# Performance work log

Hardware: AMD Instinct MI355X
Metric: run time of the kernel (lower is better)

The kernel has to match this reference:

```python
import jax, jax.numpy as jnp
import numpy as np

N = 100000
IN_CH, HID_CH, OUT_CH = 128, 128, 64
E = 1600000


def gcn_layer(x, W, b, src, dst, num_nodes):
    """PyG GCNConv: add self-loops, symmetric deg^-1/2 normalization,
    x' = D^-1/2 (A+I) D^-1/2 (x W) + b."""
    # degrees including self-loops (deg = 1 + in-degree with unit edge weights)
    ones = jnp.ones(dst.shape[0], dtype=x.dtype)
    deg = jnp.ones(num_nodes, dtype=x.dtype).at[dst].add(ones)
    dinv = jax.lax.rsqrt(deg)
    h = x @ W  # [N, out_dim] -- transform before propagate (PyG order)
    # neighbor messages
    norm = dinv[src] * dinv[dst]                      # [E]
    msg = h[src] * norm[:, None]                      # [E, out_dim] (traffic-bound)
    agg = jax.ops.segment_sum(msg, dst, num_segments=num_nodes)
    # self-loop contribution: norm_ii = dinv[i]^2
    agg = agg + h * (dinv * dinv)[:, None]
    return agg + b


def setup_inputs() -> dict:
    key = jax.random.key(0)
    ks = jax.random.split(key, 7)
    x = jax.random.normal(ks[0], (N, IN_CH), dtype=jnp.float32)
    edge_index = jax.random.randint(ks[1], (2, E), 0, N, dtype=jnp.int64)
    # Glorot-style init like PyG GCNConv
    W1 = jax.random.normal(ks[2], (IN_CH, HID_CH), dtype=jnp.float32) * (1.0 / np.sqrt(IN_CH))
    b1 = jnp.zeros((HID_CH,), dtype=jnp.float32)
    W2 = jax.random.normal(ks[3], (HID_CH, OUT_CH), dtype=jnp.float32) * (1.0 / np.sqrt(HID_CH))
    b2 = jnp.zeros((OUT_CH,), dtype=jnp.float32)
    return {"x": x, "edge_index": edge_index, "W1": W1, "b1": b1, "W2": W2, "b2": b2}


def reference(x, edge_index, W1, b1, W2, b2):
    src, dst = edge_index[0], edge_index[1]
    h = gcn_layer(x, W1, b1, src, dst, N)
    h = jax.nn.relu(h)  # dropout is identity in eval mode
    out = gcn_layer(h, W2, b2, src, dst, N)
    return out
```

## Files before the change

kernel.cpp:

```cpp
#include <hip/hip_runtime.h>
#include <hip/hip_fp16.h>

#define NNODES 100000
#define NEDGES 1600000
#define IN_C   128
#define HID_C  128
#define OUT_C  64

#define CAP     64
#define OVF_MAX 4096

#define BUCKET_SHIFT 7
#define BUCKET_NODES 128
#define NB ((NNODES + BUCKET_NODES - 1) / BUCKET_NODES)
#define BCAP 3072
#define BCNT_STRIDE 16
#define EB 4096
#define NBLK_A ((NEDGES + EB - 1) / EB)
#define GB ((NNODES + 63) / 64)

typedef __attribute__((ext_vector_type(8))) _Float16 half8;
typedef __attribute__((ext_vector_type(4))) _Float16 half4;
typedef __attribute__((ext_vector_type(4))) float floatx4;

__device__ __forceinline__ long long load_idx(const void* p, long long i, int is64) {
  return is64 ? ((const long long*)p)[i] : (long long)((const int*)p)[i];
}

__global__ void zero_detect_kernel(const void* eidx, int* flag, int* bcnt,
                                   int* ovf_cnt, int* ovfA_cnt) {
  int i = blockIdx.x * 256 + threadIdx.x;
  if (i < NB * BCNT_STRIDE) bcnt[i] = 0;
  if (i == 0) { *ovf_cnt = 0; *ovfA_cnt = 0; }
  if (blockIdx.x == 0 && threadIdx.x < 64) {
    const unsigned* w = (const unsigned*)eidx;
    unsigned v = w[2 * threadIdx.x + 1];
    unsigned long long bad = __ballot(v != 0u);
    if (threadIdx.x == 0) *flag = (bad == 0ull) ? 1 : 0;
  }
}

__global__ __launch_bounds__(256) void binA_kernel(const void* __restrict__ eidx,
                                                   const int* __restrict__ flag,
                                                   int* __restrict__ bcnt,
                                                   unsigned* __restrict__ buf,
                                                   int* __restrict__ ovfA_cnt,
                                                   int2* __restrict__ ovfA) {
  __shared__ unsigned se[EB];
  __shared__ unsigned short be[EB];
  __shared__ int hist[NB];
  __shared__ int base[NB];
  __shared__ int ofs[NB];
  const int tid = threadIdx.x;
  const int e0 = blockIdx.x * EB;
  const int e1 = min(e0 + EB, NEDGES);
  const int m = e1 - e0;
  const int is64 = *flag;

  for (int b = tid; b < NB; b += 256) { hist[b] = 0; ofs[b] = 0; }
  __syncthreads();

  for (int k = tid; k < m; k += 256) {
    int e = e0 + k;
    int s = (int)load_idx(eidx, e, is64);
    int d = (int)load_idx(eidx, (long long)NEDGES + e, is64);
    int b = d >> BUCKET_SHIFT;
    se[k] = (unsigned)s | ((unsigned)(d & (BUCKET_NODES - 1)) << 17);
    be[k] = (unsigned short)b;
    atomicAdd(&hist[b], 1);
  }
  __syncthreads();

  int rot = (blockIdx.x * 131) % NB;
  for (int idx = tid; idx < NB; idx += 256) {
    int b = idx + rot;
    if (b >= NB) b -= NB;
    int h = hist[b];
    if (h > 0) base[b] = atomicAdd(&bcnt[b * BCNT_STRIDE], h);
  }
  __syncthreads();

  for (int k = tid; k < m; k += 256) {
    unsigned u = se[k];
    int b = be[k];
    int ko = atomicAdd(&ofs[b], 1);
    int slot = base[b] + ko;
    if (slot < BCAP) {
      buf[(size_t)b * BCAP + slot] = u;
    } else {
      int p = atomicAdd(ovfA_cnt, 1);
      if (p < OVF_MAX)
        ovfA[p] = make_int2((int)(u & 0x1FFFFu),
                            (b << BUCKET_SHIFT) | (int)(u >> 17));
    }
  }
}

__global__ __launch_bounds__(256) void binB_kernel(const int* __restrict__ bcnt,
                                                   const unsigned* __restrict__ buf,
                                                   const int* __restrict__ ovfA_cnt,
                                                   const int2* __restrict__ ovfA,
                                                   int* __restrict__ cnt,
                                                   float* __restrict__ dinv,
                                                   int* __restrict__ pad_csr,
                                                   int* __restrict__ ovf_cnt,
                                                   int2* __restrict__ ovf) {
  __shared__ int pad[BUCKET_NODES * CAP];
  __shared__ int lcnt[BUCKET_NODES];
  const int b = blockIdx.x;
  const int tid = threadIdx.x;
  const int node0 = b << BUCKET_SHIFT;

  if (tid < BUCKET_NODES) lcnt[tid] = 0;
  __syncthreads();

  const int n = min(bcnt[b * BCNT_STRIDE], BCAP);
  for (int k = tid; k < n; k += 256) {
    unsigned u = buf[(size_t)b * BCAP + k];
    int s = (int)(u & 0x1FFFFu);
    int dl = (int)(u >> 17);
    int slot = atomicAdd(&lcnt[dl], 1);
    if (slot < CAP) {
      pad[dl * CAP + slot] = s;
    } else {
      int p = atomicAdd(ovf_cnt, 1);
      if (p < OVF_MAX) ovf[p] = make_int2(s, node0 + dl);
    }
  }
  int na = min(*ovfA_cnt, OVF_MAX);
  for (int t = tid; t < na; t += 256) {
    int2 p = ovfA[t];
    if ((p.y >> BUCKET_SHIFT) == b) {
      int dl = p.y & (BUCKET_NODES - 1);
      int slot = atomicAdd(&lcnt[dl], 1);
      if (slot < CAP) {
        pad[dl * CAP + slot] = p.x;
      } else {
        int q = atomicAdd(ovf_cnt, 1);
        if (q < OVF_MAX) ovf[q] = make_int2(p.x, p.y);
      }
    }
  }
  __syncthreads();

  constexpr int I4PN = CAP / 4;
  for (int q = tid; q < BUCKET_NODES * I4PN; q += 256) {
    int dl = q / I4PN;
    int gn = node0 + dl;
    if (gn < NNODES) {
      int c = (q % I4PN) * 4;
      *(int4*)&pad_csr[(size_t)gn * CAP + c] = *(const int4*)&pad[dl * CAP + c];
    }
  }
  if (tid < BUCKET_NODES && node0 + tid < NNODES) {
    int c = lcnt[tid];
    cnt[node0 + tid] = c;
    dinv[node0 + tid] = rsqrtf((float)(c + 1));
  }
}

__global__ __launch_bounds__(256) void gemm1_kernel(const float* __restrict__ x,
                                                    const float* __restrict__ W1,
                                                    const float* __restrict__ dinv,
                                                    _Float16* __restrict__ h1s) {
  constexpr int K = IN_C, N = HID_C, KP = K + 8;
  __shared__ alignas(16) _Float16 Alds[64 * KP];
  __shared__ alignas(16) _Float16 Wlds[N * KP];
  const int tid = threadIdx.x;
  const int row0 = blockIdx.x * 64;

  constexpr int TILES = (K / 4) * (N / 4);
  for (int tile = tid; tile < TILES; tile += 256) {
    int kt = tile & (K / 4 - 1);
    int nt = tile >> 5;
    const float* wp = &W1[(4 * kt) * N + 4 * nt];
    float4 r0 = *(const float4*)(wp);
    float4 r1 = *(const float4*)(wp + N);
    float4 r2 = *(const float4*)(wp + 2 * N);
    float4 r3 = *(const float4*)(wp + 3 * N);
    half4 c0 = {(_Float16)r0.x, (_Float16)r1.x, (_Float16)r2.x, (_Float16)r3.x};
    half4 c1 = {(_Float16)r0.y, (_Float16)r1.y, (_Float16)r2.y, (_Float16)r3.y};
    half4 c2 = {(_Float16)r0.z, (_Float16)r1.z, (_Float16)r2.z, (_Float16)r3.z};
    half4 c3 = {(_Float16)r0.w, (_Float16)r1.w, (_Float16)r2.w, (_Float16)r3.w};
    *(half4*)&Wlds[(4 * nt + 0) * KP + 4 * kt] = c0;
    *(half4*)&Wlds[(4 * nt + 1) * KP + 4 * kt] = c1;
    *(half4*)&Wlds[(4 * nt + 2) * KP + 4 * kt] = c2;
    *(half4*)&Wlds[(4 * nt + 3) * KP + 4 * kt] = c3;
  }
  constexpr int F4PR = K / 4;
  for (int idx = tid; idx < 64 * F4PR; idx += 256) {
    int lr = idx >> 5;
    int c4 = (idx & 31) * 4;
    int gr = row0 + lr;
    if (gr > NNODES - 1) gr = NNODES - 1;
    float4 v = *(const float4*)&x[(size_t)gr * K + c4];
    half4 h = {(_Float16)v.x, (_Float16)v.y, (_Float16)v.z, (_Float16)v.w};
    *(half4*)&Alds[lr * KP + c4] = h;
  }
  __syncthreads();

  const int w = tid >> 6;
  const int lane = tid & 63;
  const int g = lane >> 4;
  const int mi = lane & 15;
  constexpr int NT = N / 16;
  floatx4 acc[NT];
#pragma unroll
  for (int t = 0; t < NT; ++t) acc[t] = (floatx4){0.f, 0.f, 0.f, 0.f};
  const _Float16* arow = &Alds[(w * 16 + mi) * KP];
#pragma unroll
  for (int ks = 0; ks < K / 32; ++ks) {
    half8 a = *(const half8*)(arow + ks * 32 + g * 8);
#pragma unroll
    for (int t = 0; t < NT; ++t) {
      half8 b = *(const half8*)&Wlds[(t * 16 + mi) * KP + ks * 32 + g * 8];
      acc[t] = __builtin_amdgcn_mfma_f32_16x16x32_f16(a, b, acc[t], 0, 0, 0);
    }
  }
#pragma unroll
  for (int r = 0; r < 4; ++r) {
    int grow = row0 + w * 16 + 4 * g + r;
    if (grow < NNODES) {
      float s = dinv[grow];
      _Float16* orow = h1s + (size_t)grow * N + mi;
#pragma unroll
      for (int t = 0; t < NT; ++t) orow[t * 16] = (_Float16)(acc[t][r] * s);
    }
  }
}

struct F8 {
  float x0, x1, x2, x3, x4, x5, x6, x7;
};

__device__ __forceinline__ void add_h8(F8& a, const __half* p) {
  int4 r = *(const int4*)p;
  const __half2* h = (const __half2*)&r;
  float2 f0 = __half22float2(h[0]);
  float2 f1 = __half22float2(h[1]);
  float2 f2 = __half22float2(h[2]);
  float2 f3 = __half22float2(h[3]);
  a.x0 += f0.x; a.x1 += f0.y; a.x2 += f1.x; a.x3 += f1.y;
  a.x4 += f2.x; a.x5 += f2.y; a.x6 += f3.x; a.x7 += f3.y;
}

__global__ __launch_bounds__(512) void gather1_gemm2_kernel(
    const int* __restrict__ cnt, const int* __restrict__ pad_csr,
    const float* __restrict__ dinv, const __half* __restrict__ Hs1,
    const float* __restrict__ b1, const float* __restrict__ W2,
    const int* __restrict__ ovf_cnt, const int2* __restrict__ ovf,
    _Float16* __restrict__ h2s) {
  constexpr int K = HID_C, N = OUT_C, KP = K + 8;
  __shared__ alignas(16) _Float16 Hl[64 * KP];
  __shared__ alignas(16) _Float16 W2l[N * KP];
  const int tid = threadIdx.x;
  const int node0 = blockIdx.x * 64;

  constexpr int TILES = (K / 4) * (N / 4);
  for (int tile = tid; tile < TILES; tile += 512) {
    int kt = tile & (K / 4 - 1);
    int nt = tile >> 5;
    const float* wp = &W2[(4 * kt) * N + 4 * nt];
    float4 r0 = *(const float4*)(wp);
    float4 r1 = *(const float4*)(wp + N);
    float4 r2 = *(const float4*)(wp + 2 * N);
    float4 r3 = *(const float4*)(wp + 3 * N);
    half4 c0 = {(_Float16)r0.x, (_Float16)r1.x, (_Float16)r2.x, (_Float16)r3.x};
    half4 c1 = {(_Float16)r0.y, (_Float16)r1.y, (_Float16)r2.y, (_Float16)r3.y};
    half4 c2 = {(_Float16)r0.z, (_Float16)r1.z, (_Float16)r2.z, (_Float16)r3.z};
    half4 c3 = {(_Float16)r0.w, (_Float16)r1.w, (_Float16)r2.w, (_Float16)r3.w};
    *(half4*)&W2l[(4 * nt + 0) * KP + 4 * kt] = c0;
    *(half4*)&W2l[(4 * nt + 1) * KP + 4 * kt] = c1;
    *(half4*)&W2l[(4 * nt + 2) * KP + 4 * kt] = c2;
    *(half4*)&W2l[(4 * nt + 3) * KP + 4 * kt] = c3;
  }

  const int il = tid >> 3;
  const int c16 = (tid & 7) * 16;
  const int i = node0 + il;

  float o[16];
#pragma unroll
  for (int q = 0; q < 16; ++q) o[q] = 0.f;

  if (i < NNODES) {
    const float di = dinv[i];
    const int deg = cnt[i];
    const int beg = i * CAP;
    const int end = beg + min(deg, CAP);
    const int* __restrict__ lst = pad_csr;
    const __half* __restrict__ Hb = Hs1 + c16;

    F8 a0l = {}, a0h = {}, a1l = {}, a1h = {};
    {
      const __half* p = Hb + (size_t)i * K;
      add_h8(a0l, p);
      add_h8(a0h, p + 8);
    }
    int j = beg;
    for (; j + 8 <= end; j += 8) {
      int4 sa = *(const int4*)&lst[j];
      int4 sb = *(const int4*)&lst[j + 4];
      const __half* p0 = Hb + (size_t)sa.x * K;
      const __half* p1 = Hb + (size_t)sa.y * K;
      const __half* p2 = Hb + (size_t)sa.z * K;
      const __half* p3 = Hb + (size_t)sa.w * K;
      add_h8(a0l, p0); add_h8(a0h, p0 + 8);
      add_h8(a1l, p1); add_h8(a1h, p1 + 8);
      add_h8(a0l, p2); add_h8(a0h, p2 + 8);
      add_h8(a1l, p3); add_h8(a1h, p3 + 8);
      const __half* p4 = Hb + (size_t)sb.x * K;
      const __half* p5 = Hb + (size_t)sb.y * K;
      const __half* p6 = Hb + (size_t)sb.z * K;
      const __half* p7 = Hb + (size_t)sb.w * K;
      add_h8(a0l, p4); add_h8(a0h, p4 + 8);
      add_h8(a1l, p5); add_h8(a1h, p5 + 8);
      add_h8(a0l, p6); add_h8(a0h, p6 + 8);
      add_h8(a1l, p7); add_h8(a1h, p7 + 8);
    }
    for (; j + 2 <= end; j += 2) {
      const __half* p0 = Hb + (size_t)lst[j] * K;
      const __half* p1 = Hb + (size_t)lst[j + 1] * K;
      add_h8(a0l, p0); add_h8(a0h, p0 + 8);
      add_h8(a1l, p1); add_h8(a1h, p1 + 8);
    }
    if (j < end) {
      const __half* p0 = Hb + (size_t)lst[j] * K;
      add_h8(a0l, p0); add_h8(a0h, p0 + 8);
    }
    if (deg > CAP) {
      int nv = min(*ovf_cnt, OVF_MAX);
      for (int t = 0; t < nv; ++t) {
        int2 p = ovf[t];
        if (p.y == i) {
          const __half* q = Hb + (size_t)p.x * K;
          add_h8(a0l, q); add_h8(a0h, q + 8);
        }
      }
    }
    float4 bb0 = *(const float4*)&b1[c16];
    float4 bb1 = *(const float4*)&b1[c16 + 4];
    float4 bb2 = *(const float4*)&b1[c16 + 8];
    float4 bb3 = *(const float4*)&b1[c16 + 12];
    o[0] = fmaf(a0l.x0 + a1l.x0, di, bb0.x);
    o[1] = fmaf(a0l.x1 + a1l.x1, di, bb0.y);
    o[2] = fmaf(a0l.x2 + a1l.x2, di, bb0.z);
    o[3] = fmaf(a0l.x3 + a1l.x3, di, bb0.w);
    o[4] = fmaf(a0l.x4 + a1l.x4, di, bb1.x);
    o[5] = fmaf(a0l.x5 + a1l.x5, di, bb1.y);
    o[6] = fmaf(a0l.x6 + a1l.x6, di, bb1.z);
    o[7] = fmaf(a0l.x7 + a1l.x7, di, bb1.w);
    o[8] = fmaf(a0h.x0 + a1h.x0, di, bb2.x);
    o[9] = fmaf(a0h.x1 + a1h.x1, di, bb2.y);
    o[10] = fmaf(a0h.x2 + a1h.x2, di, bb2.z);
    o[11] = fmaf(a0h.x3 + a1h.x3, di, bb2.w);
    o[12] = fmaf(a0h.x4 + a1h.x4, di, bb3.x);
    o[13] = fmaf(a0h.x5 + a1h.x5, di, bb3.y);
    o[14] = fmaf(a0h.x6 + a1h.x6, di, bb3.z);
    o[15] = fmaf(a0h.x7 + a1h.x7, di, bb3.w);
#pragma unroll
    for (int q = 0; q < 16; ++q) o[q] = o[q] > 0.f ? o[q] : 0.f;
  }
  {
    half8 hv0 = {(_Float16)o[0], (_Float16)o[1], (_Float16)o[2], (_Float16)o[3],
                 (_Float16)o[4], (_Float16)o[5], (_Float16)o[6], (_Float16)o[7]};
    half8 hv1 = {(_Float16)o[8], (_Float16)o[9], (_Float16)o[10], (_Float16)o[11],
                 (_Float16)o[12], (_Float16)o[13], (_Float16)o[14], (_Float16)o[15]};
    *(half8*)&Hl[il * KP + c16] = hv0;
    *(half8*)&Hl[il * KP + c16 + 8] = hv1;
  }
  __syncthreads();

  const int w = tid >> 6;
  const int lane = tid & 63;
  const int g = lane >> 4;
  const int mi = lane & 15;
  const int wrow = (w & 3) * 16;
  const int wcol = (w >> 2) * 32;

  floatx4 acc[2];
  acc[0] = (floatx4){0.f, 0.f, 0.f, 0.f};
  acc[1] = (floatx4){0.f, 0.f, 0.f, 0.f};
  const _Float16* arow = &Hl[(wrow + mi) * KP];
#pragma unroll
  for (int ks = 0; ks < K / 32; ++ks) {
    half8 a = *(const half8*)(arow + ks * 32 + g * 8);
#pragma unroll
    for (int t = 0; t < 2; ++t) {
      half8 b = *(const half8*)&W2l[(wcol + t * 16 + mi) * KP + ks * 32 + g * 8];
      acc[t] = __builtin_amdgcn_mfma_f32_16x16x32_f16(a, b, acc[t], 0, 0, 0);
    }
  }
#pragma unroll
  for (int r = 0; r < 4; ++r) {
    int grow = node0 + wrow + 4 * g + r;
    if (grow < NNODES) {
      float s = dinv[grow];
      _Float16* orow = h2s + (size_t)grow * N + wcol + mi;
#pragma unroll
      for (int t = 0; t < 2; ++t) orow[t * 16] = (_Float16)(acc[t][r] * s);
    }
  }
}

__global__ __launch_bounds__(256) void gather2_kernel(
    const int* __restrict__ cnt, const int* __restrict__ pad_csr,
    const float* __restrict__ dinv, const __half* __restrict__ Hs2,
    const float* __restrict__ b2, const int* __restrict__ ovf_cnt,
    const int2* __restrict__ ovf, float* __restrict__ Out) {
  constexpr int C = OUT_C;
  constexpr int TPN = C / 16;
  int gid = blockIdx.x * 256 + threadIdx.x;
  int i = gid / TPN;
  int c16 = (gid % TPN) * 16;
  if (i >= NNODES) return;

  const float di = dinv[i];
  const int deg = cnt[i];
  const int beg = i * CAP;
  const int end = beg + min(deg, CAP);
  const int* __restrict__ lst = pad_csr;
  const __half* __restrict__ Hb = Hs2 + c16;

  F8 a0l = {}, a0h = {}, a1l = {}, a1h = {};
  {
    const __half* p = Hb + (size_t)i * C;
    add_h8(a0l, p);
    add_h8(a0h, p + 8);
  }
  int j = beg;
  for (; j + 8 <= end; j += 8) {
    int4 sa = *(const int4*)&lst[j];
    int4 sb = *(const int4*)&lst[j + 4];
    const __half* p0 = Hb + (size_t)sa.x * C;
    const __half* p1 = Hb + (size_t)sa.y * C;
    const __half* p2 = Hb + (size_t)sa.z * C;
    const __half* p3 = Hb + (size_t)sa.w * C;
    add_h8(a0l, p0); add_h8(a0h, p0 + 8);
    add_h8(a1l, p1); add_h8(a1h, p1 + 8);
    add_h8(a0l, p2); add_h8(a0h, p2 + 8);
    add_h8(a1l, p3); add_h8(a1h, p3 + 8);
    const __half* p4 = Hb + (size_t)sb.x * C;
    const __half* p5 = Hb + (size_t)sb.y * C;
    const __half* p6 = Hb + (size_t)sb.z * C;
    const __half* p7 = Hb + (size_t)sb.w * C;
    add_h8(a0l, p4); add_h8(a0h, p4 + 8);
    add_h8(a1l, p5); add_h8(a1h, p5 + 8);
    add_h8(a0l, p6); add_h8(a0h, p6 + 8);
    add_h8(a1l, p7); add_h8(a1h, p7 + 8);
  }
  for (; j + 2 <= end; j += 2) {
    const __half* p0 = Hb + (size_t)lst[j] * C;
    const __half* p1 = Hb + (size_t)lst[j + 1] * C;
    add_h8(a0l, p0); add_h8(a0h, p0 + 8);
    add_h8(a1l, p1); add_h8(a1h, p1 + 8);
  }
  if (j < end) {
    const __half* p0 = Hb + (size_t)lst[j] * C;
    add_h8(a0l, p0); add_h8(a0h, p0 + 8);
  }
  if (deg > CAP) {
    int nv = min(*ovf_cnt, OVF_MAX);
    for (int t = 0; t < nv; ++t) {
      int2 p = ovf[t];
      if (p.y == i) {
        const __half* q = Hb + (size_t)p.x * C;
        add_h8(a0l, q); add_h8(a0h, q + 8);
      }
    }
  }

  float4 bb0 = *(const float4*)&b2[c16];
  float4 bb1 = *(const float4*)&b2[c16 + 4];
  float4 bb2 = *(const float4*)&b2[c16 + 8];
  float4 bb3 = *(const float4*)&b2[c16 + 12];
  float* O = Out + (size_t)i * C + c16;
  *(float4*)O = make_float4(fmaf(a0l.x0 + a1l.x0, di, bb0.x),
                            fmaf(a0l.x1 + a1l.x1, di, bb0.y),
                            fmaf(a0l.x2 + a1l.x2, di, bb0.z),
                            fmaf(a0l.x3 + a1l.x3, di, bb0.w));
  *(float4*)(O + 4) = make_float4(fmaf(a0l.x4 + a1l.x4, di, bb1.x),
                                  fmaf(a0l.x5 + a1l.x5, di, bb1.y),
                                  fmaf(a0l.x6 + a1l.x6, di, bb1.z),
                                  fmaf(a0l.x7 + a1l.x7, di, bb1.w));
  *(float4*)(O + 8) = make_float4(fmaf(a0h.x0 + a1h.x0, di, bb2.x),
                                  fmaf(a0h.x1 + a1h.x1, di, bb2.y),
                                  fmaf(a0h.x2 + a1h.x2, di, bb2.z),
                                  fmaf(a0h.x3 + a1h.x3, di, bb2.w));
  *(float4*)(O + 12) = make_float4(fmaf(a0h.x4 + a1h.x4, di, bb3.x),
                                   fmaf(a0h.x5 + a1h.x5, di, bb3.y),
                                   fmaf(a0h.x6 + a1h.x6, di, bb3.z),
                                   fmaf(a0h.x7 + a1h.x7, di, bb3.w));
}

extern "C" void kernel_launch(void* const* d_in, const int* in_sizes, int n_in,
                              void* d_out, int out_size, void* d_ws, size_t ws_size,
                              hipStream_t stream) {
  const float* x = (const float*)d_in[0];
  const void* eidx = d_in[1];
  const float* W1 = (const float*)d_in[2];
  const float* b1 = (const float*)d_in[3];
  const float* W2 = (const float*)d_in[4];
  const float* b2 = (const float*)d_in[5];
  float* out = (float*)d_out;
  char* ws = (char*)d_ws;

  int*      flag     = (int*)(ws + 0);
  int*      ovf_cnt  = (int*)(ws + 512);
  int*      ovfA_cnt = (int*)(ws + 1024);
  int*      bcnt     = (int*)(ws + 1536);
  int*      cnt      = (int*)(ws + 52224);
  float*    dinv     = (float*)(ws + 452608);
  int2*     ovf      = (int2*)(ws + 852992);
  int2*     ovfA     = (int2*)(ws + 885760);
  unsigned* buf      = (unsigned*)(ws + 918528);
  int*      pad_csr  = (int*)(ws + 10528256);
  _Float16* h1s      = (_Float16*)(ws + 36128256);
  _Float16* h2s      = (_Float16*)(ws + 61728256);

  zero_detect_kernel<<<(NB * BCNT_STRIDE + 255) / 256, 256, 0, stream>>>(
      eidx, flag, bcnt, ovf_cnt, ovfA_cnt);
  binA_kernel<<<NBLK_A, 256, 0, stream>>>(eidx, flag, bcnt, buf, ovfA_cnt, ovfA);
  binB_kernel<<<NB, 256, 0, stream>>>(bcnt, buf, ovfA_cnt, ovfA, cnt, dinv,
                                      pad_csr, ovf_cnt, ovf);
  gemm1_kernel<<<GB, 256, 0, stream>>>(x, W1, dinv, h1s);
  gather1_gemm2_kernel<<<GB, 512, 0, stream>>>(cnt, pad_csr, dinv,
                                               (const __half*)h1s, b1, W2,
                                               ovf_cnt, ovf, h2s);
  gather2_kernel<<<(NNODES * (OUT_C / 16) + 255) / 256, 256, 0, stream>>>(
      cnt, pad_csr, dinv, (const __half*)h2s, b2, ovf_cnt, ovf, out);
}
```

Before: 281.6 us.

## Split fused gather/GEMM2, pre-transpose weights once, halve column work per gather block

Weight transposition and fp16 conversion move into the prep kernel, so the GEMM kernels load pre-transposed fp16 tiles instead of redoing the transpose in every block. The fused gather1+GEMM2 kernel is split into a standalone gather1 that writes the hidden activations to global memory and a separate MFMA gemm2 kernel. Both gather kernels now give each block half of the feature columns, interleaving the halves across adjacent blocks, which is meant to improve cache locality and occupancy. The binning kernels move to 512 threads per block. The split adds a round trip of the hidden matrix through global memory and one more launch.

```diff
diff --git a/kernel.cpp b/kernel.cpp
--- a/kernel.cpp
+++ b/kernel.cpp
@@ -27,8 +27,12 @@
   return is64 ? ((const long long*)p)[i] : (long long)((const int*)p)[i];
 }
 
-__global__ void zero_detect_kernel(const void* eidx, int* flag, int* bcnt,
-                                   int* ovf_cnt, int* ovfA_cnt) {
+__global__ void prep_kernel(const void* eidx, int* flag, int* bcnt,
+                            int* ovf_cnt, int* ovfA_cnt,
+                            const float* __restrict__ W1,
+                            const float* __restrict__ W2,
+                            _Float16* __restrict__ Wt1,
+                            _Float16* __restrict__ Wt2) {
   int i = blockIdx.x * 256 + threadIdx.x;
   if (i < NB * BCNT_STRIDE) bcnt[i] = 0;
   if (i == 0) { *ovf_cnt = 0; *ovfA_cnt = 0; }
@@ -38,9 +42,18 @@
     unsigned long long bad = __ballot(v != 0u);
     if (threadIdx.x == 0) *flag = (bad == 0ull) ? 1 : 0;
   }
-}
-
-__global__ __launch_bounds__(256) void binA_kernel(const void* __restrict__ eidx,
+  const int stride = gridDim.x * 256;
+  for (int t = i; t < IN_C * HID_C; t += stride) {
+    int n = t >> 7, k = t & 127;
+    Wt1[t] = (_Float16)W1[k * HID_C + n];
+  }
+  for (int t = i; t < HID_C * OUT_C; t += stride) {
+    int n = t >> 7, k = t & 127;
+    Wt2[t] = (_Float16)W2[k * OUT_C + n];
+  }
+}
+
+__global__ __launch_bounds__(512) void binA_kernel(const void* __restrict__ eidx,
                                                    const int* __restrict__ flag,
                                                    int* __restrict__ bcnt,
                                                    unsigned* __restrict__ buf,
@@ -57,10 +70,10 @@
   const int m = e1 - e0;
   const int is64 = *flag;
 
-  for (int b = tid; b < NB; b += 256) { hist[b] = 0; ofs[b] = 0; }
-  __syncthreads();
-
-  for (int k = tid; k < m; k += 256) {
+  for (int b = tid; b < NB; b += 512) { hist[b] = 0; ofs[b] = 0; }
+  __syncthreads();
+
+  for (int k = tid; k < m; k += 512) {
     int e = e0 + k;
     int s = (int)load_idx(eidx, e, is64);
     int d = (int)load_idx(eidx, (long long)NEDGES + e, is64);
@@ -72,7 +85,7 @@
   __syncthreads();
 
   int rot = (blockIdx.x * 131) % NB;
-  for (int idx = tid; idx < NB; idx += 256) {
+  for (int idx = tid; idx < NB; idx += 512) {
     int b = idx + rot;
     if (b >= NB) b -= NB;
     int h = hist[b];
@@ -80,7 +93,7 @@
   }
   __syncthreads();
 
-  for (int k = tid; k < m; k += 256) {
+  for (int k = tid; k < m; k += 512) {
     unsigned u = se[k];
     int b = be[k];
     int ko = atomicAdd(&ofs[b], 1);
@@ -96,7 +109,7 @@
   }
 }
 
-__global__ __launch_bounds__(256) void binB_kernel(const int* __restrict__ bcnt,
+__global__ __launch_bounds__(512) void binB_kernel(const int* __restrict__ bcnt,
                                                    const unsigned* __restrict__ buf,
                                                    const int* __restrict__ ovfA_cnt,
                                                    const int2* __restrict__ ovfA,
@@ -115,7 +128,7 @@
   __syncthreads();
 
   const int n = min(bcnt[b * BCNT_STRIDE], BCAP);
-  for (int k = tid; k < n; k += 256) {
+  for (int k = tid; k < n; k += 512) {
     unsigned u = buf[(size_t)b * BCAP + k];
     int s = (int)(u & 0x1FFFFu);
     int dl = (int)(u >> 17);
@@ -128,7 +141,7 @@
     }
   }
   int na = min(*ovfA_cnt, OVF_MAX);
-  for (int t = tid; t < na; t += 256) {
+  for (int t = tid; t < na; t += 512) {
     int2 p = ovfA[t];
     if ((p.y >> BUCKET_SHIFT) == b) {
       int dl = p.y & (BUCKET_NODES - 1);
@@ -144,7 +157,7 @@
   __syncthreads();
 
   constexpr int I4PN = CAP / 4;
-  for (int q = tid; q < BUCKET_NODES * I4PN; q += 256) {
+  for (int q = tid; q < BUCKET_NODES * I4PN; q += 512) {
     int dl = q / I4PN;
     int gn = node0 + dl;
     if (gn < NNODES) {
@@ -160,7 +173,7 @@
 }
 
 __global__ __launch_bounds__(256) void gemm1_kernel(const float* __restrict__ x,
-                                                    const float* __restrict__ W1,
+                                                    const _Float16* __restrict__ Wt1,
                                                     const float* __restrict__ dinv,
                                                     _Float16* __restrict__ h1s) {
   constexpr int K = IN_C, N = HID_C, KP = K + 8;
@@ -169,23 +182,9 @@
   const int tid = threadIdx.x;
   const int row0 = blockIdx.x * 64;
 
-  constexpr int TILES = (K / 4) * (N / 4);
-  for (int tile = tid; tile < TILES; tile += 256) {
-    int kt = tile & (K / 4 - 1);
-    int nt = tile >> 5;
-    const float* wp = &W1[(4 * kt) * N + 4 * nt];
-    float4 r0 = *(const float4*)(wp);
-    float4 r1 = *(const float4*)(wp + N);
-    float4 r2 = *(const float4*)(wp + 2 * N);
-    float4 r3 = *(const float4*)(wp + 3 * N);
-    half4 c0 = {(_Float16)r0.x, (_Float16)r1.x, (_Float16)r2.x, (_Float16)r3.x};
-    half4 c1 = {(_Float16)r0.y, (_Float16)r1.y, (_Float16)r2.y, (_Float16)r3.y};
-    half4 c2 = {(_Float16)r0.z, (_Float16)r1.z, (_Float16)r2.z, (_Float16)r3.z};
-    half4 c3 = {(_Float16)r0.w, (_Float16)r1.w, (_Float16)r2.w, (_Float16)r3.w};
-    *(half4*)&Wlds[(4 * nt + 0) * KP + 4 * kt] = c0;
-    *(half4*)&Wlds[(4 * nt + 1) * KP + 4 * kt] = c1;
-    *(half4*)&Wlds[(4 * nt + 2) * KP + 4 * kt] = c2;
-    *(half4*)&Wlds[(4 * nt + 3) * KP + 4 * kt] = c3;
+  for (int idx = tid; idx < N * (K / 8); idx += 256) {
+    int n = idx >> 4, k16 = idx & 15;
+    *(int4*)&Wlds[n * KP + k16 * 8] = *(const int4*)&Wt1[n * K + k16 * 8];
   }
   constexpr int F4PR = K / 4;
   for (int idx = tid; idx < 64 * F4PR; idx += 256) {
@@ -229,6 +228,59 @@
   }
 }
 
+__global__ __launch_bounds__(256) void gemm2_kernel(const _Float16* __restrict__ hid,
+                                                    const _Float16* __restrict__ Wt2,
+                                                    const float* __restrict__ dinv,
+                                                    _Float16* __restrict__ h2s) {
+  constexpr int K = HID_C, N = OUT_C, KP = K + 8;
+  __shared__ alignas(16) _Float16 Alds[64 * KP];
+  __shared__ alignas(16) _Float16 Wlds[N * KP];
+  const int tid = threadIdx.x;
+  const int row0 = blockIdx.x * 64;
+
+  for (int idx = tid; idx < N * (K / 8); idx += 256) {
+    int n = idx >> 4, k16 = idx & 15;
+    *(int4*)&Wlds[n * KP + k16 * 8] = *(const int4*)&Wt2[n * K + k16 * 8];
+  }
+  for (int idx = tid; idx < 64 * (K / 8); idx += 256) {
+    int lr = idx >> 4, k16 = idx & 15;
+    int gr = row0 + lr;
+    if (gr > NNODES - 1) gr = NNODES - 1;
+    *(int4*)&Alds[lr * KP + k16 * 8] =
+        *(const int4*)&hid[(size_t)gr * K + k16 * 8];
+  }
+  __syncthreads();
+
+  const int w = tid >> 6;
+  const int lane = tid & 63;
+  const int g = lane >> 4;
+  const int mi = lane & 15;
+  constexpr int NT = N / 16;
+  floatx4 acc[NT];
+#pragma unroll
+  for (int t = 0; t < NT; ++t) acc[t] = (floatx4){0.f, 0.f, 0.f, 0.f};
+  const _Float16* arow = &Alds[(w * 16 + mi) * KP];
+#pragma unroll
+  for (int ks = 0; ks < K / 32; ++ks) {
+    half8 a = *(const half8*)(arow + ks * 32 + g * 8);
+#pragma unroll
+    for (int t = 0; t < NT; ++t) {
+      half8 b = *(const half8*)&Wlds[(t * 16 + mi) * KP + ks * 32 + g * 8];
+      acc[t] = __builtin_amdgcn_mfma_f32_16x16x32_f16(a, b, acc[t], 0, 0, 0);
+    }
+  }
+#pragma unroll
+  for (int r = 0; r < 4; ++r) {
+    int grow = row0 + w * 16 + 4 * g + r;
+    if (grow < NNODES) {
+      float s = dinv[grow];
+      _Float16* orow = h2s + (size_t)grow * N + mi;
+#pragma unroll
+      for (int t = 0; t < NT; ++t) orow[t * 16] = (_Float16)(acc[t][r] * s);
+    }
+  }
+}
+
 struct F8 {
   float x0, x1, x2, x3, x4, x5, x6, x7;
 };
@@ -244,163 +296,110 @@
   a.x4 += f2.x; a.x5 += f2.y; a.x6 += f3.x; a.x7 += f3.y;
 }
 
-__global__ __launch_bounds__(512) void gather1_gemm2_kernel(
+__global__ __launch_bounds__(256) void gather1_kernel(
     const int* __restrict__ cnt, const int* __restrict__ pad_csr,
     const float* __restrict__ dinv, const __half* __restrict__ Hs1,
-    const float* __restrict__ b1, const float* __restrict__ W2,
-    const int* __restrict__ ovf_cnt, const int2* __restrict__ ovf,
-    _Float16* __restrict__ h2s) {
-  constexpr int K = HID_C, N = OUT_C, KP = K + 8;
-  __shared__ alignas(16) _Float16 Hl[64 * KP];
-  __shared__ alignas(16) _Float16 W2l[N * KP];
-  const int tid = threadIdx.x;
-  const int node0 = blockIdx.x * 64;
-
-  constexpr int TILES = (K / 4) * (N / 4);
-  for (int tile = tid; tile < TILES; tile += 512) {
-    int kt = tile & (K / 4 - 1);
-    int nt = tile >> 5;
-    const float* wp = &W2[(4 * kt) * N + 4 * nt];
-    float4 r0 = *(const float4*)(wp);
-    float4 r1 = *(const float4*)(wp + N);
-    float4 r2 = *(const float4*)(wp + 2 * N);
-    float4 r3 = *(const float4*)(wp + 3 * N);
-    half4 c0 = {(_Float16)r0.x, (_Float16)r1.x, (_Float16)r2.x, (_Float16)r3.x};
-    half4 c1 = {(_Float16)r0.y, (_Float16)r1.y, (_Float16)r2.y, (_Float16)r3.y};
-    half4 c2 = {(_Float16)r0.z, (_Float16)r1.z, (_Float16)r2.z, (_Float16)r3.z};
-    half4 c3 = {(_Float16)r0.w, (_Float16)r1.w, (_Float16)r2.w, (_Float16)r3.w};
-    *(half4*)&W2l[(4 * nt + 0) * KP + 4 * kt] = c0;
-    *(half4*)&W2l[(4 * nt + 1) * KP + 4 * kt] = c1;
-    *(half4*)&W2l[(4 * nt + 2) * KP + 4 * kt] = c2;
-    *(half4*)&W2l[(4 * nt + 3) * KP + 4 * kt] = c3;
-  }
-
-  const int il = tid >> 3;
-  const int c16 = (tid & 7) * 16;
-  const int i = node0 + il;
-
-  float o[16];
-#pragma unroll
-  for (int q = 0; q < 16; ++q) o[q] = 0.f;
-
-  if (i < NNODES) {
-    const float di = dinv[i];
-    const int deg = cnt[i];
-    const int beg = i * CAP;
-    const int end = beg + min(deg, CAP);
-    const int* __restrict__ lst = pad_csr;
-    const __half* __restrict__ Hb = Hs1 + c16;
-
-    F8 a0l = {}, a0h = {}, a1l = {}, a1h = {};
-    {
-      const __half* p = Hb + (size_t)i * K;
-      add_h8(a0l, p);
-      add_h8(a0h, p + 8);
-    }
-    int j = beg;
-    for (; j + 8 <= end; j += 8) {
-      int4 sa = *(const int4*)&lst[j];
-      int4 sb = *(const int4*)&lst[j + 4];
-      const __half* p0 = Hb + (size_t)sa.x * K;
-      const __half* p1 = Hb + (size_t)sa.y * K;
-      const __half* p2 = Hb + (size_t)sa.z * K;
-      const __half* p3 = Hb + (size_t)sa.w * K;
-      add_h8(a0l, p0); add_h8(a0h, p0 + 8);
-      add_h8(a1l, p1); add_h8(a1h, p1 + 8);
-      add_h8(a0l, p2); add_h8(a0h, p2 + 8);
-      add_h8(a1l, p3); add_h8(a1h, p3 + 8);
-      const __half* p4 = Hb + (size_t)sb.x * K;
-      const __half* p5 = Hb + (size_t)sb.y * K;
-      const __half* p6 = Hb + (size_t)sb.z * K;
-      const __half* p7 = Hb + (size_t)sb.w * K;
-      add_h8(a0l, p4); add_h8(a0h, p4 + 8);
-      add_h8(a1l, p5); add_h8(a1h, p5 + 8);
-      add_h8(a0l, p6); add_h8(a0h, p6 + 8);
-      add_h8(a1l, p7); add_h8(a1h, p7 + 8);
-    }
-    for (; j + 2 <= end; j += 2) {
-      const __half* p0 = Hb + (size_t)lst[j] * K;
-      const __half* p1 = Hb + (size_t)lst[j + 1] * K;
-      add_h8(a0l, p0); add_h8(a0h, p0 + 8);
-      add_h8(a1l, p1); add_h8(a1h, p1 + 8);
-    }
-    if (j < end) {
-      const __half* p0 = Hb + (size_t)lst[j] * K;
-      add_h8(a0l, p0); add_h8(a0h, p0 + 8);
-    }
-    if (deg > CAP) {
-      int nv = min(*ovf_cnt, OVF_MAX);
-      for (int t = 0; t < nv; ++t) {
-        int2 p = ovf[t];
-        if (p.y == i) {
-          const __half* q = Hb + (size_t)p.x * K;
-          add_h8(a0l, q); add_h8(a0h, q + 8);
-        }
+    const float* __restrict__ b1, const int* __restrict__ ovf_cnt,
+    const int2* __restrict__ ovf, _Float16* __restrict__ hidden) {
+  constexpr int C = HID_C;
+  const int half = blockIdx.x & 1;
+  const int tile = blockIdx.x >> 1;
+  const int il = threadIdx.x >> 2;
+  const int c16 = half * 64 + (threadIdx.x & 3) * 16;
+  const int i = tile * 64 + il;
+  if (i >= NNODES) return;
+
+  const float di = dinv[i];
+  const int deg = cnt[i];
+  const int beg = i * CAP;
+  const int end = beg + min(deg, CAP);
+  const int* __restrict__ lst = pad_csr;
+  const __half* __restrict__ Hb = Hs1 + c16;
+
+  F8 a0l = {}, a0h = {}, a1l = {}, a1h = {};
+  {
+    const __half* p = Hb + (size_t)i * C;
+    add_h8(a0l, p);
+    add_h8(a0h, p + 8);
+  }
+  int j = beg;
+  for (; j + 8 <= end; j += 8) {
+    int4 sa = *(const int4*)&lst[j];
+    int4 sb = *(const int4*)&lst[j + 4];
+    const __half* p0 = Hb + (size_t)sa.x * C;
+    const __half* p1 = Hb + (size_t)sa.y * C;
+    const __half* p2 = Hb + (size_t)sa.z * C;
+    const __half* p3 = Hb + (size_t)sa.w * C;
+    add_h8(a0l, p0); add_h8(a0h, p0 + 8);
+    add_h8(a1l, p1); add_h8(a1h, p1 + 8);
+    add_h8(a0l, p2); add_h8(a0h, p2 + 8);
+    add_h8(a1l, p3); add_h8(a1h, p3 + 8);
+    const __half* p4 = Hb + (size_t)sb.x * C;
+    const __half* p5 = Hb + (size_t)sb.y * C;
+    const __half* p6 = Hb + (size_t)sb.z * C;
+    const __half* p7 = Hb + (size_t)sb.w * C;
+    add_h8(a0l, p4); add_h8(a0h, p4 + 8);
+    add_h8(a1l, p5); add_h8(a1h, p5 + 8);
+    add_h8(a0l, p6); add_h8(a0h, p6 + 8);
+    add_h8(a1l, p7); add_h8(a1h, p7 + 8);
+  }
+  for (; j + 2 <= end; j += 2) {
+    const __half* p0 = Hb + (size_t)lst[j] * C;
+    const __half* p1 = Hb + (size_t)lst[j + 1] * C;
+    add_h8(a0l, p0); add_h8(a0h, p0 + 8);
+    add_h8(a1l, p1); add_h8(a1h, p1 + 8);
+  }
+  if (j < end) {
+    const __half* p0 = Hb + (size_t)lst[j] * C;
+    add_h8(a0l, p0); add_h8(a0h, p0 + 8);
+  }
+  if (deg > CAP) {
+    int nv = min(*ovf_cnt, OVF_MAX);
+    for (int t = 0; t < nv; ++t) {
+      int2 p = ovf[t];
+      if (p.y == i) {
+        const __half* q = Hb + (size_t)p.x * C;
+        add_h8(a0l, q); add_h8(a0h, q + 8);
       }
     }
-    float4 bb0 = *(const float4*)&b1[c16];
-    float4 bb1 = *(const float4*)&b1[c16 + 4];
-    float4 bb2 = *(const float4*)&b1[c16 + 8];
-    float4 bb3 = *(const float4*)&b1[c16 + 12];
-    o[0] = fmaf(a0l.x0 + a1l.x0, di, bb0.x);
-    o[1] = fmaf(a0l.x1 + a1l.x1, di, bb0.y);
-    o[2] = fmaf(a0l.x2 + a1l.x2, di, bb0.z);
-    o[3] = fmaf(a0l.x3 + a1l.x3, di, bb0.w);
-    o[4] = fmaf(a0l.x4 + a1l.x4, di, bb1.x);
-    o[5] = fmaf(a0l.x5 + a1l.x5, di, bb1.y);
-    o[6] = fmaf(a0l.x6 + a1l.x6, di, bb1.z);
-    o[7] = fmaf(a0l.x7 + a1l.x7, di, bb1.w);
-    o[8] = fmaf(a0h.x0 + a1h.x0, di, bb2.x);
-    o[9] = fmaf(a0h.x1 + a1h.x1, di, bb2.y);
-    o[10] = fmaf(a0h.x2 + a1h.x2, di, bb2.z);
-    o[11] = fmaf(a0h.x3 + a1h.x3, di, bb2.w);
-    o[12] = fmaf(a0h.x4 + a1h.x4, di, bb3.x);
-    o[13] = fmaf(a0h.x5 + a1h.x5, di, bb3.y);
-    o[14] = fmaf(a0h.x6 + a1h.x6, di, bb3.z);
-    o[15] = fmaf(a0h.x7 + a1h.x7, di, bb3.w);
-#pragma unroll
-    for (int q = 0; q < 16; ++q) o[q] = o[q] > 0.f ? o[q] : 0.f;
-  }
-  {
-    half8 hv0 = {(_Float16)o[0], (_Float16)o[1], (_Float16)o[2], (_Float16)o[3],
-                 (_Float16)o[4], (_Float16)o[5], (_Float16)o[6], (_Float16)o[7]};
-    half8 hv1 = {(_Float16)o[8], (_Float16)o[9], (_Float16)o[10], (_Float16)o[11],
-                 (_Float16)o[12], (_Float16)o[13], (_Float16)o[14], (_Float16)o[15]};
-    *(half8*)&Hl[il * KP + c16] = hv0;
-    *(half8*)&Hl[il * KP + c16 + 8] = hv1;
-  }
-  __syncthreads();
-
-  const int w = tid >> 6;
-  const int lane = tid & 63;
-  const int g = lane >> 4;
-  const int mi = lane & 15;
-  const int wrow = (w & 3) * 16;
-  const int wcol = (w >> 2) * 32;
-
-  floatx4 acc[2];
-  acc[0] = (floatx4){0.f, 0.f, 0.f, 0.f};
-  acc[1] = (floatx4){0.f, 0.f, 0.f, 0.f};
-  const _Float16* arow = &Hl[(wrow + mi) * KP];
-#pragma unroll
-  for (int ks = 0; ks < K / 32; ++ks) {
-    half8 a = *(const half8*)(arow + ks * 32 + g * 8);
-#pragma unroll
-    for (int t = 0; t < 2; ++t) {
-      half8 b = *(const half8*)&W2l[(wcol + t * 16 + mi) * KP + ks * 32 + g * 8];
-      acc[t] = __builtin_amdgcn_mfma_f32_16x16x32_f16(a, b, acc[t], 0, 0, 0);
-    }
-  }
-#pragma unroll
-  for (int r = 0; r < 4; ++r) {
-    int grow = node0 + wrow + 4 * g + r;
-    if (grow < NNODES) {
-      float s = dinv[grow];
-      _Float16* orow = h2s + (size_t)grow * N + wcol + mi;
-#pragma unroll
-      for (int t = 0; t < 2; ++t) orow[t * 16] = (_Float16)(acc[t][r] * s);
-    }
-  }
+  }
+
+  float4 bb0 = *(const float4*)&b1[c16];
+  float4 bb1 = *(const float4*)&b1[c16 + 4];
+  float4 bb2 = *(const float4*)&b1[c16 + 8];
+  float4 bb3 = *(const float4*)&b1[c16 + 12];
+  float o0 = fmaf(a0l.x0 + a1l.x0, di, bb0.x);
+  float o1 = fmaf(a0l.x1 + a1l.x1, di, bb0.y);
+  float o2 = fmaf(a0l.x2 + a1l.x2, di, bb0.z);
+  float o3 = fmaf(a0l.x3 + a1l.x3, di, bb0.w);
+  float o4 = fmaf(a0l.x4 + a1l.x4, di, bb1.x);
+  float o5 = fmaf(a0l.x5 + a1l.x5, di, bb1.y);
+  float o6 = fmaf(a0l.x6 + a1l.x6, di, bb1.z);
+  float o7 = fmaf(a0l.x7 + a1l.x7, di, bb1.w);
+  float o8 = fmaf(a0h.x0 + a1h.x0, di, bb2.x);
+  float o9 = fmaf(a0h.x1 + a1h.x1, di, bb2.y);
+  float o10 = fmaf(a0h.x2 + a1h.x2, di, bb2.z);
+  float o11 = fmaf(a0h.x3 + a1h.x3, di, bb2.w);
+  float o12 = fmaf(a0h.x4 + a1h.x4, di, bb3.x);
+  float o13 = fmaf(a0h.x5 + a1h.x5, di, bb3.y);
+  float o14 = fmaf(a0h.x6 + a1h.x6, di, bb3.z);
+  float o15 = fmaf(a0h.x7 + a1h.x7, di, bb3.w);
+  o0 = o0 > 0.f ? o0 : 0.f;   o1 = o1 > 0.f ? o1 : 0.f;
+  o2 = o2 > 0.f ? o2 : 0.f;   o3 = o3 > 0.f ? o3 : 0.f;
+  o4 = o4 > 0.f ? o4 : 0.f;   o5 = o5 > 0.f ? o5 : 0.f;
+  o6 = o6 > 0.f ? o6 : 0.f;   o7 = o7 > 0.f ? o7 : 0.f;
+  o8 = o8 > 0.f ? o8 : 0.f;   o9 = o9 > 0.f ? o9 : 0.f;
+  o10 = o10 > 0.f ? o10 : 0.f; o11 = o11 > 0.f ? o11 : 0.f;
+  o12 = o12 > 0.f ? o12 : 0.f; o13 = o13 > 0.f ? o13 : 0.f;
+  o14 = o14 > 0.f ? o14 : 0.f; o15 = o15 > 0.f ? o15 : 0.f;
+
+  _Float16* Out = hidden + (size_t)i * C + c16;
+  half8 hv0 = {(_Float16)o0, (_Float16)o1, (_Float16)o2, (_Float16)o3,
+               (_Float16)o4, (_Float16)o5, (_Float16)o6, (_Float16)o7};
+  half8 hv1 = {(_Float16)o8, (_Float16)o9, (_Float16)o10, (_Float16)o11,
+               (_Float16)o12, (_Float16)o13, (_Float16)o14, (_Float16)o15};
+  *(half8*)Out = hv0;
+  *(half8*)(Out + 8) = hv1;
 }
 
 __global__ __launch_bounds__(256) void gather2_kernel(
@@ -409,10 +408,11 @@
     const float* __restrict__ b2, const int* __restrict__ ovf_cnt,
     const int2* __restrict__ ovf, float* __restrict__ Out) {
   constexpr int C = OUT_C;
-  constexpr int TPN = C / 16;
-  int gid = blockIdx.x * 256 + threadIdx.x;
-  int i = gid / TPN;
-  int c16 = (gid % TPN) * 16;
+  const int half = blockIdx.x & 1;
+  const int tile = blockIdx.x >> 1;
+  const int il = threadIdx.x >> 1;
+  const int c16 = half * 32 + (threadIdx.x & 1) * 16;
+  const int i = tile * 128 + il;
   if (i >= NNODES) return;
 
   const float di = dinv[i];
@@ -513,20 +513,24 @@
   float*    dinv     = (float*)(ws + 452608);
   int2*     ovf      = (int2*)(ws + 852992);
   int2*     ovfA     = (int2*)(ws + 885760);
-  unsigned* buf      = (unsigned*)(ws + 918528);
-  int*      pad_csr  = (int*)(ws + 10528256);
-  _Float16* h1s      = (_Float16*)(ws + 36128256);
-  _Float16* h2s      = (_Float16*)(ws + 61728256);
-
-  zero_detect_kernel<<<(NB * BCNT_STRIDE + 255) / 256, 256, 0, stream>>>(
-      eidx, flag, bcnt, ovf_cnt, ovfA_cnt);
-  binA_kernel<<<NBLK_A, 256, 0, stream>>>(eidx, flag, bcnt, buf, ovfA_cnt, ovfA);
-  binB_kernel<<<NB, 256, 0, stream>>>(bcnt, buf, ovfA_cnt, ovfA, cnt, dinv,
+  _Float16* Wt1      = (_Float16*)(ws + 918528);
+  _Float16* Wt2      = (_Float16*)(ws + 951296);
+  unsigned* buf      = (unsigned*)(ws + 968192);
+  int*      pad_csr  = (int*)(ws + 10577920);
+  _Float16* h1s      = (_Float16*)(ws + 36178432);
+  _Float16* hidden   = (_Float16*)(ws + 61778944);
+  _Float16* h2s      = h1s;
+
+  prep_kernel<<<(NB * BCNT_STRIDE + 255) / 256, 256, 0, stream>>>(
+      eidx, flag, bcnt, ovf_cnt, ovfA_cnt, W1, W2, Wt1, Wt2);
+  binA_kernel<<<NBLK_A, 512, 0, stream>>>(eidx, flag, bcnt, buf, ovfA_cnt, ovfA);
+  binB_kernel<<<NB, 512, 0, stream>>>(bcnt, buf, ovfA_cnt, ovfA, cnt, dinv,
                                       pad_csr, ovf_cnt, ovf);
-  gemm1_kernel<<<GB, 256, 0, stream>>>(x, W1, dinv, h1s);
-  gather1_gemm2_kernel<<<GB, 512, 0, stream>>>(cnt, pad_csr, dinv,
-                                               (const __half*)h1s, b1, W2,
-                                               ovf_cnt, ovf, h2s);
-  gather2_kernel<<<(NNODES * (OUT_C / 16) + 255) / 256, 256, 0, stream>>>(
+  gemm1_kernel<<<GB, 256, 0, stream>>>(x, Wt1, dinv, h1s);
+  gather1_kernel<<<2 * GB, 256, 0, stream>>>(cnt, pad_csr, dinv,
+                                             (const __half*)h1s, b1,
+                                             ovf_cnt, ovf, hidden);
+  gemm2_kernel<<<GB, 256, 0, stream>>>(hidden, Wt2, dinv, h2s);
+  gather2_kernel<<<2 * ((NNODES + 127) / 128), 256, 0, stream>>>(
       cnt, pad_csr, dinv, (const __half*)h2s, b2, ovf_cnt, ovf, out);
 }
```

After: 293.0 us. +4.0%, slower.
